# Kernel optimization log

Hardware: AMD Instinct MI355X
Metric: run time of the kernel (lower is better)

## Reference

```python
import jax, jax.numpy as jnp
import numpy as np

EPS = 1e-5  # torch BatchNorm2d and LayerNorm default eps

def conv1x1(x, w, b=None):
    # x: [N,Cin,H,W], w: [Cout,Cin]
    y = jnp.einsum('nchw,oc->nohw', x, w)
    if b is not None:
        y = y + b[None, :, None, None]
    return y

def bn_inf(x, g, b, m, v):
    # inference-mode BatchNorm2d with running stats
    s = g / jnp.sqrt(v + EPS)
    return x * s[None, :, None, None] + (b - m * s)[None, :, None, None]

def silu(x):
    return x * jax.nn.sigmoid(x)

def conv_block(x, w, g, b, m, v):
    # Conv(c1,c2,1,1): 1x1 conv (no bias) + BN + SiLU
    return silu(bn_inf(conv1x1(x, w), g, b, m, v))

def setup_inputs() -> dict:
    key = jax.random.key(0)
    N, C, H, W = 8, 64, 256, 256
    ks = jax.random.split(key, 8)
    sc = 1.0 / np.sqrt(C)
    d = {}
    d['rgb_fea'] = jax.random.normal(ks[0], (N, C, H, W), jnp.float32)
    d['ir_fea']  = jax.random.normal(ks[1], (N, C, H, W), jnp.float32)
    d['conv_w']  = jax.random.normal(ks[2], (C, C), jnp.float32) * sc
    d['conv_b']  = jax.random.normal(ks[3], (C,), jnp.float32) * 0.1
    d['key_w']   = jax.random.normal(ks[4], (1, C), jnp.float32) * sc
    d['key_g'] = jnp.ones((1,), jnp.float32); d['key_b'] = jnp.zeros((1,), jnp.float32)
    d['key_m'] = jnp.zeros((1,), jnp.float32); d['key_v'] = jnp.ones((1,), jnp.float32)
    d['val_w']   = jax.random.normal(ks[5], (C, C), jnp.float32) * sc
    d['val_g'] = jnp.ones((C,), jnp.float32); d['val_b'] = jnp.zeros((C,), jnp.float32)
    d['val_m'] = jnp.zeros((C,), jnp.float32); d['val_v'] = jnp.ones((C,), jnp.float32)
    d['convb_w'] = jax.random.normal(ks[6], (C, C), jnp.float32) * sc
    d['half_w']  = jax.random.normal(ks[7], (1, 2), jnp.float32) * 0.7
    d['half_g'] = jnp.ones((1,), jnp.float32); d['half_b'] = jnp.zeros((1,), jnp.float32)
    d['half_m'] = jnp.zeros((1,), jnp.float32); d['half_v'] = jnp.ones((1,), jnp.float32)
    d['ln_g'] = jnp.ones((C,), jnp.float32); d['ln_b'] = jnp.zeros((C,), jnp.float32)
    return d

def reference(rgb_fea, ir_fea, conv_w, conv_b, key_w, key_g, key_b, key_m, key_v,
              val_w, val_g, val_b, val_m, val_v, convb_w,
              half_w, half_g, half_b, half_m, half_v, ln_g, ln_b):
    N, C, H, W = rgb_fea.shape

    def side(x):
        xc = conv1x1(x, conv_w, conv_b)                         # [N,C,H,W]
        avg = jax.nn.softmax(xc.mean(axis=(2, 3)), axis=1)      # [N,C]
        mx  = jax.nn.softmax(xc.max(axis=(2, 3)), axis=1)       # [N,C]
        k = conv_block(x, key_w, key_g, key_b, key_m, key_v)    # [N,1,H,W]
        k = jax.nn.softmax(k.reshape(N, H * W), axis=1)          # [N,HW]
        v = conv_block(x, val_w, val_g, val_b, val_m, val_v)    # [N,C,H,W]
        return avg, mx, k, v.reshape(N, C, H * W)

    r_avg, r_max, r_key, r_val = side(rgb_fea)
    i_avg, i_max, i_key, i_val = side(ir_fea)

    def ln(z):  # LayerNorm over channel dim of [N,C] (the [C,1,1] norm)
        mu = z.mean(axis=1, keepdims=True)
        var = ((z - mu) ** 2).mean(axis=1, keepdims=True)
        return (z - mu) / jnp.sqrt(var + EPS) * ln_g + ln_b

    def fuse(other_val, my_avg, my_max, my_key, me):
        fea = jnp.einsum('nce,ne->nc', other_val, my_key)        # value @ key -> [N,C]
        gate = jax.nn.sigmoid(ln(fea @ convb_w.T))[:, :, None, None]  # [N,C,1,1]
        avgm = jnp.einsum('nc,nce->ne', my_avg, other_val).reshape(N, 1, H, W)
        maxm = jnp.einsum('nc,nce->ne', my_max, other_val).reshape(N, 1, H, W)
        cat = jnp.concatenate([avgm, maxm], axis=1)              # [N,2,H,W]
        half = conv_block(cat, half_w, half_g, half_b, half_m, half_v)  # [N,1,H,W]
        return gate * half + me

    out_rgb = fuse(i_val, r_avg, r_max, r_key, rgb_fea)
    out_ir  = fuse(r_val, i_avg, i_max, i_key, ir_fea)
    return (out_rgb, out_ir)
```

## Files before the change

kernel.cpp:

```cpp
#include <hip/hip_runtime.h>
#include <math.h>

constexpr int Nn  = 8;
constexpr int Cc  = 64;
constexpr int HWp = 65536;
constexpr int TPB = 256;
constexpr int PPT = 4;
constexpr int PIXB = TPB * PPT;
constexpr int CHUNKS = HWp / PIXB;

__device__ inline unsigned fkey(float f) {
  unsigned u = __float_as_uint(f);
  return (u & 0x80000000u) ? ~u : (u | 0x80000000u);
}
__device__ inline float funkey(unsigned k) {
  return __uint_as_float((k & 0x80000000u) ? (k & 0x7fffffffu) : ~k);
}
__device__ inline float wmax(float v) {
#pragma unroll
  for (int m = 32; m; m >>= 1) v = fmaxf(v, __shfl_xor(v, m, 64));
  return v;
}
__device__ inline float wsum(float v) {
#pragma unroll
  for (int m = 32; m; m >>= 1) v += __shfl_xor(v, m, 64);
  return v;
}
__device__ inline float silu_(float z) { return z / (1.f + __expf(-z)); }

__global__ __launch_bounds__(TPB) void k1_stats(
    const float* __restrict__ xrgb, const float* __restrict__ xir,
    const float* __restrict__ conv_w, const float* __restrict__ conv_b,
    const float* __restrict__ key_w, const float* __restrict__ key_g,
    const float* __restrict__ key_b, const float* __restrict__ key_m,
    const float* __restrict__ key_v,
    float* __restrict__ kpre, unsigned* __restrict__ mxk,
    float* __restrict__ smo, float* __restrict__ ksum)
{
  const int side = blockIdx.z, n = blockIdx.y, chunk = blockIdx.x;
  const float* x = (side ? xir : xrgb) + (size_t)n * Cc * HWp;
  const int sn = side * Nn + n;
  const float ks = key_g[0] * rsqrtf(key_v[0] + 1e-5f);
  const float kb = key_b[0] - key_m[0] * ks;
  const int lane = threadIdx.x & 63;

  float mxacc = -1e30f;
  float smacc = 0.f;
  float keacc = 0.f;

  float* kp = kpre + (size_t)sn * HWp;
  const int e0 = chunk * PIXB + threadIdx.x;
#pragma unroll 1
  for (int i = 0; i < PPT; i++) {
    const int e = e0 + i * TPB;
    float xv[64];
#pragma unroll
    for (int c = 0; c < 64; c++) xv[c] = x[(size_t)c * HWp + e];
    float kd = 0.f;
#pragma unroll
    for (int c = 0; c < 64; c++) kd += key_w[c] * xv[c];
    float ka = silu_(ks * kd + kb);
    kp[e] = ka;
    keacc += __expf(ka);
#pragma unroll 4
    for (int o = 0; o < 64; o++) {
      float acc = conv_b[o];
#pragma unroll
      for (int c = 0; c < 64; c++) acc += conv_w[o * 64 + c] * xv[c];
      float m = wmax(acc);
      float s = wsum(acc);
      if (lane == o) { mxacc = fmaxf(mxacc, m); smacc += s; }
    }
  }
  atomicMax(&mxk[sn * 64 + lane], fkey(mxacc));
  atomicAdd(&smo[sn * 64 + lane], smacc);
  float kes = wsum(keacc);
  if (lane == 0) atomicAdd(&ksum[sn], kes);
}

__global__ void k3_fin(const float* __restrict__ smo, const unsigned* __restrict__ mxk,
                       const float* __restrict__ val_g, const float* __restrict__ val_b,
                       const float* __restrict__ val_m, const float* __restrict__ val_v,
                       float* __restrict__ avg, float* __restrict__ mxs,
                       float* __restrict__ vs_arr, float* __restrict__ vb_arr)
{
  const int sn = blockIdx.x, o = threadIdx.x;
  if (sn == 0) {
    float s = val_g[o] * rsqrtf(val_v[o] + 1e-5f);
    vs_arr[o] = s;
    vb_arr[o] = val_b[o] - val_m[o] * s;
  }
  float lm = smo[sn * 64 + o] * (1.f / HWp);
  float M = wmax(lm);
  float E = __expf(lm - M);
  float S = wsum(E);
  avg[sn * 64 + o] = E / S;
  float mm = funkey(mxk[sn * 64 + o]);
  M = wmax(mm);
  E = __expf(mm - M);
  S = wsum(E);
  mxs[sn * 64 + o] = E / S;
}

__global__ __launch_bounds__(TPB) void k4_val(
    const float* __restrict__ xrgb, const float* __restrict__ xir,
    const float* __restrict__ val_w,
    const float* __restrict__ vs_arr, const float* __restrict__ vb_arr,
    const float* __restrict__ avg, const float* __restrict__ mxs,
    const float* __restrict__ kpre, const float* __restrict__ ksum,
    const float* __restrict__ half_w, const float* __restrict__ half_g,
    const float* __restrict__ half_b, const float* __restrict__ half_m,
    const float* __restrict__ half_v,
    float* __restrict__ halfb, float* __restrict__ fea)
{
  const int me = blockIdx.z, n = blockIdx.y, chunk = blockIdx.x;
  const float* xo = (me ? xrgb : xir) + (size_t)n * Cc * HWp;
  const int sn = me * Nn + n;
  const float kinv = 1.f / ksum[sn];
  const float* kp = kpre + (size_t)sn * HWp;
  const float hs = half_g[0] * rsqrtf(half_v[0] + 1e-5f);
  const float hb = half_b[0] - half_m[0] * hs;
  const float hw0 = half_w[0], hw1 = half_w[1];
  float* hp = halfb + (size_t)sn * HWp;
  const int lane = threadIdx.x & 63;

  float feap = 0.f;

  const int e0 = chunk * PIXB + threadIdx.x;
#pragma unroll 1
  for (int i = 0; i < PPT; i++) {
    const int e = e0 + i * TPB;
    float xv[64];
#pragma unroll
    for (int c = 0; c < 64; c++) xv[c] = xo[(size_t)c * HWp + e];
    const float kw = __expf(kp[e]) * kinv;
    float am = 0.f, mm = 0.f;
#pragma unroll 4
    for (int o = 0; o < 64; o++) {
      float acc = 0.f;
#pragma unroll
      for (int c = 0; c < 64; c++) acc += val_w[o * 64 + c] * xv[c];
      float v = silu_(vs_arr[o] * acc + vb_arr[o]);
      am += avg[sn * 64 + o] * v;
      mm += mxs[sn * 64 + o] * v;
      float s = wsum(v * kw);
      if (lane == o) feap += s;
    }
    hp[e] = silu_(hs * (hw0 * am + hw1 * mm) + hb);
  }
  atomicAdd(&fea[sn * 64 + lane], feap);
}

__global__ void k5_gate(const float* __restrict__ fea, const float* __restrict__ convb_w,
                        const float* __restrict__ ln_g, const float* __restrict__ ln_b,
                        float* __restrict__ gate)
{
  const int sn = blockIdx.x, o = threadIdx.x;
  float z = 0.f;
#pragma unroll
  for (int c = 0; c < 64; c++) z += convb_w[o * 64 + c] * fea[sn * 64 + c];
  float mu = wsum(z) * (1.f / 64);
  float d = z - mu;
  float var = wsum(d * d) * (1.f / 64);
  float g = d * rsqrtf(var + 1e-5f) * ln_g[o] + ln_b[o];
  gate[sn * 64 + o] = 1.f / (1.f + __expf(-g));
}

__global__ __launch_bounds__(256) void k6_out(
    const float* __restrict__ xrgb, const float* __restrict__ xir,
    const float* __restrict__ gate, const float* __restrict__ halfb,
    float* __restrict__ out)
{
  const size_t t = (size_t)blockIdx.x * 256 + threadIdx.x;
  const int e4 = (int)(t & (HWp / 4 - 1));
  size_t r = t >> 14;
  const int c = (int)(r & 63); r >>= 6;
  const int n = (int)(r & 7);
  const int me = (int)(r >> 3);
  const float* x = me ? xir : xrgb;
  const float4 xv = ((const float4*)x)[(((size_t)n * 64 + c) << 14) + e4];
  const float g = gate[(me * 8 + n) * 64 + c];
  const float4 h = ((const float4*)halfb)[((size_t)(me * 8 + n) << 14) + e4];
  float4 ov;
  ov.x = g * h.x + xv.x;
  ov.y = g * h.y + xv.y;
  ov.z = g * h.z + xv.z;
  ov.w = g * h.w + xv.w;
  ((float4*)out)[t] = ov;
}

extern "C" void kernel_launch(void* const* d_in, const int* in_sizes, int n_in,
                              void* d_out, int out_size, void* d_ws, size_t ws_size,
                              hipStream_t stream)
{
  const float* xrgb   = (const float*)d_in[0];
  const float* xir    = (const float*)d_in[1];
  const float* conv_w = (const float*)d_in[2];
  const float* conv_b = (const float*)d_in[3];
  const float* key_w  = (const float*)d_in[4];
  const float* key_g  = (const float*)d_in[5];
  const float* key_b  = (const float*)d_in[6];
  const float* key_m  = (const float*)d_in[7];
  const float* key_v  = (const float*)d_in[8];
  const float* val_w  = (const float*)d_in[9];
  const float* val_g  = (const float*)d_in[10];
  const float* val_b  = (const float*)d_in[11];
  const float* val_m  = (const float*)d_in[12];
  const float* val_v  = (const float*)d_in[13];
  const float* convb_w= (const float*)d_in[14];
  const float* half_w = (const float*)d_in[15];
  const float* half_g = (const float*)d_in[16];
  const float* half_b = (const float*)d_in[17];
  const float* half_m = (const float*)d_in[18];
  const float* half_v = (const float*)d_in[19];
  const float* ln_g   = (const float*)d_in[20];
  const float* ln_b   = (const float*)d_in[21];

  float* ws      = (float*)d_ws;
  float* kpre    = ws;
  float* halfb   = kpre + 2 * Nn * HWp;
  float* smo     = halfb + 2 * Nn * HWp;
  unsigned* mxk  = (unsigned*)(smo + 1024);
  float* ksum    = (float*)(mxk + 1024);
  float* fea     = ksum + 16;
  float* avg     = fea + 1024;
  float* mxs     = avg + 1024;
  float* gate    = mxs + 1024;
  float* vs_arr  = gate + 1024;
  float* vb_arr  = vs_arr + 64;

  hipMemsetAsync(smo, 0, (size_t)(1024 + 1024 + 16 + 1024) * sizeof(float), stream);

  dim3 gHeavy(CHUNKS, Nn, 2);
  k1_stats<<<gHeavy, TPB, 0, stream>>>(xrgb, xir, conv_w, conv_b, key_w, key_g, key_b,
                                       key_m, key_v, kpre, mxk, smo, ksum);
  k3_fin<<<16, 64, 0, stream>>>(smo, mxk, val_g, val_b, val_m, val_v,
                                avg, mxs, vs_arr, vb_arr);
  k4_val<<<gHeavy, TPB, 0, stream>>>(xrgb, xir, val_w, vs_arr, vb_arr, avg, mxs, kpre,
                                     ksum, half_w, half_g, half_b, half_m, half_v,
                                     halfb, fea);
  k5_gate<<<16, 64, 0, stream>>>(fea, convb_w, ln_g, ln_b, gate);
  k6_out<<<(2 * Nn * Cc * HWp / 4) / 256, 256, 0, stream>>>(xrgb, xir, gate, halfb,
                                                            (float*)d_out);
}
```

Baseline: 882.5 us.

## Use fp16 MFMA for the 1x1 conv GEMMs in stats and value kernels

Replaces the per-thread scalar 64x64 channel matmuls and the wave-wide shuffle reductions per output channel with MFMA 16x16x32 fp16 instructions. Each wave now processes strips of 16 pixels, with inputs and weights converted to half precision and per-lane accumulators reduced once at the end. The conv bias is moved out of the max/sum accumulation and added later in the finalisation kernel, which is exact because bias commutes with both max and mean. Work is regridded so that each wave covers a contiguous pixel range. This trades fp32 accuracy for fp16 inputs to the matmul.

```diff
diff --git a/kernel.cpp b/kernel.cpp
--- a/kernel.cpp
+++ b/kernel.cpp
@@ -5,9 +5,14 @@
 constexpr int Cc  = 64;
 constexpr int HWp = 65536;
 constexpr int TPB = 256;
-constexpr int PPT = 4;
-constexpr int PIXB = TPB * PPT;
-constexpr int CHUNKS = HWp / PIXB;
+constexpr int BPS = 64;
+constexpr int WPS = BPS * 4;
+constexpr int PXW = HWp / WPS;
+constexpr int SPW = PXW / 16;
+
+typedef _Float16 f16;
+typedef _Float16 f16x8 __attribute__((ext_vector_type(8)));
+typedef float    f32x4 __attribute__((ext_vector_type(4)));
 
 __device__ inline unsigned fkey(float f) {
   unsigned u = __float_as_uint(f);
@@ -30,55 +35,106 @@
 
 __global__ __launch_bounds__(TPB) void k1_stats(
     const float* __restrict__ xrgb, const float* __restrict__ xir,
-    const float* __restrict__ conv_w, const float* __restrict__ conv_b,
+    const float* __restrict__ conv_w,
     const float* __restrict__ key_w, const float* __restrict__ key_g,
     const float* __restrict__ key_b, const float* __restrict__ key_m,
     const float* __restrict__ key_v,
     float* __restrict__ kpre, unsigned* __restrict__ mxk,
     float* __restrict__ smo, float* __restrict__ ksum)
 {
-  const int side = blockIdx.z, n = blockIdx.y, chunk = blockIdx.x;
+  const int side = blockIdx.z, n = blockIdx.y, blk = blockIdx.x;
+  const int wv = threadIdx.x >> 6, lane = threadIdx.x & 63;
+  const int lh = lane >> 4, lc = lane & 15;
+  const int sn = side * Nn + n;
   const float* x = (side ? xir : xrgb) + (size_t)n * Cc * HWp;
-  const int sn = side * Nn + n;
   const float ks = key_g[0] * rsqrtf(key_v[0] + 1e-5f);
   const float kb = key_b[0] - key_m[0] * ks;
-  const int lane = threadIdx.x & 63;
-
-  float mxacc = -1e30f;
-  float smacc = 0.f;
+  float* kp = kpre + (size_t)sn * HWp;
+
+  f16x8 A[4][2];
+#pragma unroll
+  for (int ob = 0; ob < 4; ob++)
+#pragma unroll
+    for (int k0 = 0; k0 < 2; k0++) {
+      const float* wr = conv_w + (16 * ob + lc) * 64 + 32 * k0 + 8 * lh;
+      float4 w0 = ((const float4*)wr)[0], w1 = ((const float4*)wr)[1];
+      A[ob][k0] = (f16x8){(f16)w0.x, (f16)w0.y, (f16)w0.z, (f16)w0.w,
+                          (f16)w1.x, (f16)w1.y, (f16)w1.z, (f16)w1.w};
+    }
+  float kw0[2][8];
+#pragma unroll
+  for (int k0 = 0; k0 < 2; k0++) {
+    const float* wr = key_w + 32 * k0 + 8 * lh;
+    float4 w0 = ((const float4*)wr)[0], w1 = ((const float4*)wr)[1];
+    kw0[k0][0] = w0.x; kw0[k0][1] = w0.y; kw0[k0][2] = w0.z; kw0[k0][3] = w0.w;
+    kw0[k0][4] = w1.x; kw0[k0][5] = w1.y; kw0[k0][6] = w1.z; kw0[k0][7] = w1.w;
+  }
+
+  f32x4 mxf[4], smf[4];
+#pragma unroll
+  for (int ob = 0; ob < 4; ob++) {
+    mxf[ob] = (f32x4){-1e30f, -1e30f, -1e30f, -1e30f};
+    smf[ob] = (f32x4){0.f, 0.f, 0.f, 0.f};
+  }
   float keacc = 0.f;
 
-  float* kp = kpre + (size_t)sn * HWp;
-  const int e0 = chunk * PIXB + threadIdx.x;
+  const int base = (blk * 4 + wv) * PXW;
 #pragma unroll 1
-  for (int i = 0; i < PPT; i++) {
-    const int e = e0 + i * TPB;
-    float xv[64];
-#pragma unroll
-    for (int c = 0; c < 64; c++) xv[c] = x[(size_t)c * HWp + e];
-    float kd = 0.f;
-#pragma unroll
-    for (int c = 0; c < 64; c++) kd += key_w[c] * xv[c];
-    float ka = silu_(ks * kd + kb);
-    kp[e] = ka;
-    keacc += __expf(ka);
-#pragma unroll 4
-    for (int o = 0; o < 64; o++) {
-      float acc = conv_b[o];
-#pragma unroll
-      for (int c = 0; c < 64; c++) acc += conv_w[o * 64 + c] * xv[c];
-      float m = wmax(acc);
-      float s = wsum(acc);
-      if (lane == o) { mxacc = fmaxf(mxacc, m); smacc += s; }
-    }
-  }
-  atomicMax(&mxk[sn * 64 + lane], fkey(mxacc));
-  atomicAdd(&smo[sn * 64 + lane], smacc);
-  float kes = wsum(keacc);
-  if (lane == 0) atomicAdd(&ksum[sn], kes);
+  for (int s = 0; s < SPW; s++) {
+    const int e = base + s * 16 + lc;
+    f16x8 B[2];
+    float keyp = 0.f;
+#pragma unroll
+    for (int k0 = 0; k0 < 2; k0++)
+#pragma unroll
+      for (int j = 0; j < 8; j++) {
+        float xf = x[(size_t)(32 * k0 + 8 * lh + j) * HWp + e];
+        B[k0][j] = (f16)xf;
+        keyp += kw0[k0][j] * xf;
+      }
+    keyp += __shfl_xor(keyp, 16, 64);
+    keyp += __shfl_xor(keyp, 32, 64);
+    if (lh == 0) {
+      float ka = silu_(ks * keyp + kb);
+      kp[e] = ka;
+      keacc += __expf(ka);
+    }
+#pragma unroll
+    for (int ob = 0; ob < 4; ob++) {
+      f32x4 t = (f32x4){0.f, 0.f, 0.f, 0.f};
+      t = __builtin_amdgcn_mfma_f32_16x16x32_f16(A[ob][0], B[0], t, 0, 0, 0);
+      t = __builtin_amdgcn_mfma_f32_16x16x32_f16(A[ob][1], B[1], t, 0, 0, 0);
+#pragma unroll
+      for (int r = 0; r < 4; r++) {
+        mxf[ob][r] = fmaxf(mxf[ob][r], t[r]);
+        smf[ob][r] += t[r];
+      }
+    }
+  }
+#pragma unroll
+  for (int ob = 0; ob < 4; ob++)
+#pragma unroll
+    for (int r = 0; r < 4; r++) {
+      float m = mxf[ob][r], sv = smf[ob][r];
+#pragma unroll
+      for (int msk = 1; msk < 16; msk <<= 1) {
+        m = fmaxf(m, __shfl_xor(m, msk, 64));
+        sv += __shfl_xor(sv, msk, 64);
+      }
+      if (lc == 0) {
+        const int o = 16 * ob + 4 * lh + r;
+        atomicMax(&mxk[sn * 64 + o], fkey(m));
+        atomicAdd(&smo[sn * 64 + o], sv);
+      }
+    }
+  float ke = keacc;
+#pragma unroll
+  for (int msk = 1; msk < 64; msk <<= 1) ke += __shfl_xor(ke, msk, 64);
+  if (lane == 0) atomicAdd(&ksum[sn], ke);
 }
 
 __global__ void k3_fin(const float* __restrict__ smo, const unsigned* __restrict__ mxk,
+                       const float* __restrict__ conv_b,
                        const float* __restrict__ val_g, const float* __restrict__ val_b,
                        const float* __restrict__ val_m, const float* __restrict__ val_v,
                        float* __restrict__ avg, float* __restrict__ mxs,
@@ -90,12 +146,13 @@
     vs_arr[o] = s;
     vb_arr[o] = val_b[o] - val_m[o] * s;
   }
-  float lm = smo[sn * 64 + o] * (1.f / HWp);
+  const float cb = conv_b[o];
+  float lm = cb + smo[sn * 64 + o] * (1.f / HWp);
   float M = wmax(lm);
   float E = __expf(lm - M);
   float S = wsum(E);
   avg[sn * 64 + o] = E / S;
-  float mm = funkey(mxk[sn * 64 + o]);
+  float mm = cb + funkey(mxk[sn * 64 + o]);
   M = wmax(mm);
   E = __expf(mm - M);
   S = wsum(E);
@@ -113,42 +170,81 @@
     const float* __restrict__ half_v,
     float* __restrict__ halfb, float* __restrict__ fea)
 {
-  const int me = blockIdx.z, n = blockIdx.y, chunk = blockIdx.x;
+  const int me = blockIdx.z, n = blockIdx.y, blk = blockIdx.x;
+  const int wv = threadIdx.x >> 6, lane = threadIdx.x & 63;
+  const int lh = lane >> 4, lc = lane & 15;
+  const int sn = me * Nn + n;
   const float* xo = (me ? xrgb : xir) + (size_t)n * Cc * HWp;
-  const int sn = me * Nn + n;
   const float kinv = 1.f / ksum[sn];
   const float* kp = kpre + (size_t)sn * HWp;
   const float hs = half_g[0] * rsqrtf(half_v[0] + 1e-5f);
   const float hb = half_b[0] - half_m[0] * hs;
   const float hw0 = half_w[0], hw1 = half_w[1];
   float* hp = halfb + (size_t)sn * HWp;
-  const int lane = threadIdx.x & 63;
-
-  float feap = 0.f;
-
-  const int e0 = chunk * PIXB + threadIdx.x;
+
+  f16x8 A[4][2];
+#pragma unroll
+  for (int ob = 0; ob < 4; ob++)
+#pragma unroll
+    for (int k0 = 0; k0 < 2; k0++) {
+      const float* wr = val_w + (16 * ob + lc) * 64 + 32 * k0 + 8 * lh;
+      float4 w0 = ((const float4*)wr)[0], w1 = ((const float4*)wr)[1];
+      A[ob][k0] = (f16x8){(f16)w0.x, (f16)w0.y, (f16)w0.z, (f16)w0.w,
+                          (f16)w1.x, (f16)w1.y, (f16)w1.z, (f16)w1.w};
+    }
+  float vsl[4][4], vbl[4][4], avl[4][4], mxl[4][4];
+#pragma unroll
+  for (int ob = 0; ob < 4; ob++)
+#pragma unroll
+    for (int r = 0; r < 4; r++) {
+      const int o = 16 * ob + 4 * lh + r;
+      vsl[ob][r] = vs_arr[o];
+      vbl[ob][r] = vb_arr[o];
+      avl[ob][r] = avg[sn * 64 + o];
+      mxl[ob][r] = mxs[sn * 64 + o];
+    }
+  f32x4 feaf[4];
+#pragma unroll
+  for (int ob = 0; ob < 4; ob++) feaf[ob] = (f32x4){0.f, 0.f, 0.f, 0.f};
+
+  const int base = (blk * 4 + wv) * PXW;
 #pragma unroll 1
-  for (int i = 0; i < PPT; i++) {
-    const int e = e0 + i * TPB;
-    float xv[64];
-#pragma unroll
-    for (int c = 0; c < 64; c++) xv[c] = xo[(size_t)c * HWp + e];
-    const float kw = __expf(kp[e]) * kinv;
+  for (int s = 0; s < SPW; s++) {
+    const int e = base + s * 16 + lc;
+    f16x8 B[2];
+#pragma unroll
+    for (int k0 = 0; k0 < 2; k0++)
+#pragma unroll
+      for (int j = 0; j < 8; j++)
+        B[k0][j] = (f16)xo[(size_t)(32 * k0 + 8 * lh + j) * HWp + e];
+    const float kwv = __expf(kp[e]) * kinv;
     float am = 0.f, mm = 0.f;
-#pragma unroll 4
-    for (int o = 0; o < 64; o++) {
-      float acc = 0.f;
-#pragma unroll
-      for (int c = 0; c < 64; c++) acc += val_w[o * 64 + c] * xv[c];
-      float v = silu_(vs_arr[o] * acc + vb_arr[o]);
-      am += avg[sn * 64 + o] * v;
-      mm += mxs[sn * 64 + o] * v;
-      float s = wsum(v * kw);
-      if (lane == o) feap += s;
-    }
-    hp[e] = silu_(hs * (hw0 * am + hw1 * mm) + hb);
-  }
-  atomicAdd(&fea[sn * 64 + lane], feap);
+#pragma unroll
+    for (int ob = 0; ob < 4; ob++) {
+      f32x4 t = (f32x4){0.f, 0.f, 0.f, 0.f};
+      t = __builtin_amdgcn_mfma_f32_16x16x32_f16(A[ob][0], B[0], t, 0, 0, 0);
+      t = __builtin_amdgcn_mfma_f32_16x16x32_f16(A[ob][1], B[1], t, 0, 0, 0);
+#pragma unroll
+      for (int r = 0; r < 4; r++) {
+        float v = silu_(vsl[ob][r] * t[r] + vbl[ob][r]);
+        am += avl[ob][r] * v;
+        mm += mxl[ob][r] * v;
+        feaf[ob][r] += v * kwv;
+      }
+    }
+    am += __shfl_xor(am, 16, 64); am += __shfl_xor(am, 32, 64);
+    mm += __shfl_xor(mm, 16, 64); mm += __shfl_xor(mm, 32, 64);
+    if (lh == 0) hp[e] = silu_(hs * (hw0 * am + hw1 * mm) + hb);
+  }
+#pragma unroll
+  for (int ob = 0; ob < 4; ob++)
+#pragma unroll
+    for (int r = 0; r < 4; r++) {
+      float sv = feaf[ob][r];
+#pragma unroll
+      for (int msk = 1; msk < 16; msk <<= 1) sv += __shfl_xor(sv, msk, 64);
+      if (lc == 0) atomicAdd(&fea[sn * 64 + 16 * ob + 4 * lh + r], sv);
+    }
 }
 
 __global__ void k5_gate(const float* __restrict__ fea, const float* __restrict__ convb_w,
@@ -231,10 +327,10 @@
 
   hipMemsetAsync(smo, 0, (size_t)(1024 + 1024 + 16 + 1024) * sizeof(float), stream);
 
-  dim3 gHeavy(CHUNKS, Nn, 2);
-  k1_stats<<<gHeavy, TPB, 0, stream>>>(xrgb, xir, conv_w, conv_b, key_w, key_g, key_b,
+  dim3 gHeavy(BPS, Nn, 2);
+  k1_stats<<<gHeavy, TPB, 0, stream>>>(xrgb, xir, conv_w, key_w, key_g, key_b,
                                        key_m, key_v, kpre, mxk, smo, ksum);
-  k3_fin<<<16, 64, 0, stream>>>(smo, mxk, val_g, val_b, val_m, val_v,
+  k3_fin<<<16, 64, 0, stream>>>(smo, mxk, conv_b, val_g, val_b, val_m, val_v,
                                 avg, mxs, vs_arr, vb_arr);
   k4_val<<<gHeavy, TPB, 0, stream>>>(xrgb, xir, val_w, vs_arr, vb_arr, avg, mxs, kpre,
                                      ksum, half_w, half_g, half_b, half_m, half_v,
```

New measurement: 715.7 us. 18.9% less time.
